# Optimization experiments

Measured on AMD Instinct MI355X. Metric: run time of the kernel, lower is better.

Reference implementation:

```python
import jax, jax.numpy as jnp
import numpy as np

D_MODEL = 768
D_STATE = 8
EXPAND = 2
D_HEAD = 64
D_CONV = 4
D_INNER = EXPAND * D_MODEL            # 1536
N_HEADS = D_INNER // D_HEAD           # 24
PARAM_DIM = 2                         # (A_freq, dt) per head per step
D_PROJ = 2 * D_INNER + N_HEADS * PARAM_DIM  # 3120
D_FF = 4 * D_MODEL
BATCH, SEQ = 2, 2048


def setup_inputs() -> dict:
    key = jax.random.key(0)
    ks = jax.random.split(key, 8)
    def s(k, shape, scale):
        return jax.random.normal(k, shape, dtype=jnp.float32) * scale
    return {
        "x": s(ks[0], (BATCH, SEQ, D_MODEL), 1.0),
        "norm1_w": jnp.ones((D_MODEL,), jnp.float32),
        "w_in": s(ks[1], (D_MODEL, D_PROJ), D_MODEL ** -0.5),
        "conv_w": s(ks[2], (D_INNER, D_CONV), D_CONV ** -0.5),
        "w_bc": s(ks[3], (D_INNER, 2 * N_HEADS * D_STATE), D_INNER ** -0.5),
        "D_skip": s(ks[4], (N_HEADS,), 1.0),
        "w_out": s(ks[5], (D_INNER, D_MODEL), D_INNER ** -0.5),
        "norm2_w": jnp.ones((D_MODEL,), jnp.float32),
        "ff_w1": s(ks[6], (D_MODEL, D_FF), D_MODEL ** -0.5),
        "ff_b1": jnp.zeros((D_FF,), jnp.float32),
        "ff_w2": s(ks[7], (D_FF, D_MODEL), D_FF ** -0.5),
        "ff_b2": jnp.zeros((D_MODEL,), jnp.float32),
    }


def _rmsnorm(x, w, eps=1e-6):
    return x * jax.lax.rsqrt(jnp.mean(x * x, axis=-1, keepdims=True) + eps) * w


def _l2norm(x, eps=1e-12):
    # normalize_bc=True: L2-normalize B/C rows over the state dim
    return x * jax.lax.rsqrt(jnp.sum(x * x, axis=-1, keepdims=True) + eps)


def _mixer(x, w_in, conv_w, w_bc, D_skip, w_out):
    Bsz, T, _ = x.shape
    proj = x @ w_in  # (B,T,3120)
    gate, vraw, params = jnp.split(proj, [D_INNER, 2 * D_INNER], axis=-1)
    # causal depthwise conv over time
    vpad = jnp.pad(vraw, ((0, 0), (D_CONV - 1, 0), (0, 0)))
    kernel = conv_w.T[:, None, :]  # (K, 1, C) for WIO, groups=C
    conv = jax.lax.conv_general_dilated(
        vpad, kernel, window_strides=(1,), padding='VALID',
        dimension_numbers=('NWC', 'WIO', 'NWC'), feature_group_count=D_INNER)
    v = jax.nn.silu(conv)  # (B,T,D_INNER)
    # B/C projections per head (normalized rows)
    bc = (v @ w_bc).reshape(Bsz, T, N_HEADS, 2, D_STATE)
    Bm = _l2norm(bc[..., 0, :])  # (B,T,H,N)
    Cm = _l2norm(bc[..., 1, :])  # (B,T,H,N)
    # LinOSS-IM discretizer: per-head time-varying frequency A and step dt
    p = params.reshape(Bsz, T, N_HEADS, PARAM_DIM)
    A = jax.nn.softplus(p[..., 0])
    dt = jax.nn.sigmoid(p[..., 1])
    S = 1.0 / (1.0 + dt * dt * A)  # implicit-midpoint Schur factor
    u = v.reshape(Bsz, T, N_HEADS, D_HEAD)
    tfirst = lambda a: jnp.moveaxis(a, 1, 0)

    def step(carry, inp):
        z, xs = carry  # each (B,H,N,P): velocity / position of the oscillator
        Bt, Ct, At, dtt, St, ut = inp
        d = dtt[..., None, None]
        a = At[..., None, None]
        s = St[..., None, None]
        bu = Bt[..., :, None] * ut[..., None, :]  # (B,H,N,P)
        z = s * (z - d * a * xs + d * bu)
        xs = xs + d * z
        y = jnp.einsum('bhn,bhnp->bhp', Ct, xs)
        return (z, xs), y

    z0 = jnp.zeros((Bsz, N_HEADS, D_STATE, D_HEAD), x.dtype)
    _, ys = jax.lax.scan(step, (z0, z0),
                         (tfirst(Bm), tfirst(Cm), tfirst(A), tfirst(dt), tfirst(S), tfirst(u)))
    y = jnp.moveaxis(ys, 0, 1)  # (B,T,H,P)
    # gate + per-head skip (D * u), then out projection
    gated = (y + D_skip[None, None, :, None] * u) * jax.nn.silu(gate).reshape(Bsz, T, N_HEADS, D_HEAD)
    return gated.reshape(Bsz, T, D_INNER) @ w_out


def reference(x, norm1_w, w_in, conv_w, w_bc, D_skip, w_out, norm2_w, ff_w1, ff_b1, ff_w2, ff_b2):
    x = x + _mixer(_rmsnorm(x, norm1_w), w_in, conv_w, w_bc, D_skip, w_out)
    h = _rmsnorm(x, norm2_w)
    return x + (jax.nn.gelu(h @ ff_w1 + ff_b1) @ ff_w2 + ff_b2)
```

## Files before the change

kernel.cpp:

```cpp
#include <hip/hip_runtime.h>

#define DMODEL 768
#define DINNER 1536
#define NHEADS 24
#define DHEAD  64
#define DSTATE 8
#define DPROJ  3120
#define DFF    3072
#define BATCH  2
#define SEQ    2048
#define BTTOT  (BATCH*SEQ)
#define NCHUNK 64
#define CT     32
#define NTBLK  8688

typedef unsigned short u16;
typedef __attribute__((ext_vector_type(8))) short bf16x8;
typedef __attribute__((ext_vector_type(4))) float f32x4;

__device__ __forceinline__ float b2f(u16 u){
  union { unsigned u; float f; } x; x.u = ((unsigned)u) << 16; return x.f;
}
__device__ __forceinline__ u16 f2b(float f){
  union { float f; unsigned u; } x; x.f = f;
  unsigned r = x.u + 0x7FFF + ((x.u >> 16) & 1);
  return (u16)(r >> 16);
}
__device__ __forceinline__ float ldin(const void* p, size_t i, bool f32){
  return f32 ? ((const float*)p)[i] : b2f(((const u16*)p)[i]);
}
__device__ __forceinline__ bool wire_f32(const u16* probe){ return probe[0] == 0; }

struct TDesc { const void* src; u16* dst; int R, C, bx, blk0; };
struct TPack { TDesc d[5]; };

__global__ __launch_bounds__(256) void pre_k(
    TPack P, const void* __restrict__ x, const void* __restrict__ w,
    u16* __restrict__ xn, const u16* __restrict__ probe)
{
  const bool f32 = wire_f32(probe);
  int bk = blockIdx.x;
  if (bk >= NTBLK){
    const size_t row = bk - NTBLK;
    float v[3]; float s = 0.f;
    #pragma unroll
    for (int i = 0; i < 3; i++){
      size_t idx = row * DMODEL + threadIdx.x + 256 * i;
      float f = ldin(x, idx, f32);
      v[i] = f; s += f * f;
    }
    #pragma unroll
    for (int o = 32; o > 0; o >>= 1) s += __shfl_xor(s, o);
    __shared__ float red[4];
    if ((threadIdx.x & 63) == 0) red[threadIdx.x >> 6] = s;
    __syncthreads();
    float tot = red[0] + red[1] + red[2] + red[3];
    float inv = rsqrtf(tot * (1.0f / DMODEL) + 1e-6f);
    #pragma unroll
    for (int i = 0; i < 3; i++){
      int c = threadIdx.x + 256 * i;
      xn[row * DMODEL + c] = f2b(v[i] * inv * ldin(w, c, f32));
    }
    return;
  }
  int s = 0;
  #pragma unroll
  for (int i = 1; i < 5; i++) if (bk >= P.d[i].blk0) s = i;
  const TDesc D = P.d[s];
  const int local = bk - D.blk0;
  const int cx = local % D.bx, ry = local / D.bx;
  const int c0 = cx * 32, r0 = ry * 32;
  const int R = D.R, C = D.C;
  __shared__ u16 tile[32][33];
  const int tx = threadIdx.x & 31, ty = threadIdx.x >> 5;
  #pragma unroll
  for (int i = 0; i < 32; i += 8){
    int r = r0 + ty + i, c = c0 + tx;
    u16 val = 0;
    if (r < R && c < C){
      size_t idx = (size_t)r * C + c;
      val = f32 ? f2b(((const float*)D.src)[idx]) : ((const u16*)D.src)[idx];
    }
    tile[ty + i][tx] = val;
  }
  __syncthreads();
  #pragma unroll
  for (int i = 0; i < 32; i += 8){
    int c = c0 + ty + i, r = r0 + tx;
    if (c < C && r < R) D.dst[(size_t)c * R + r] = tile[tx][ty + i];
  }
}

__global__ __launch_bounds__(256) void rmsnormW_k(
    const u16* __restrict__ pW, const void* __restrict__ x, const void* __restrict__ w,
    float* __restrict__ x2, u16* __restrict__ out, const u16* __restrict__ probe)
{
  const bool f32 = wire_f32(probe);
  const size_t row = blockIdx.x;
  const size_t MN = (size_t)BTTOT * DMODEL;
  float v[3]; float s = 0.f;
  #pragma unroll
  for (int i = 0; i < 3; i++){
    size_t idx = row * DMODEL + threadIdx.x + 256 * i;
    float f = ldin(x, idx, f32) + b2f(pW[idx]) + b2f(pW[MN + idx])
            + b2f(pW[2 * MN + idx]) + b2f(pW[3 * MN + idx]);
    x2[idx] = f;
    v[i] = f; s += f * f;
  }
  #pragma unroll
  for (int o = 32; o > 0; o >>= 1) s += __shfl_xor(s, o);
  __shared__ float red[4];
  if ((threadIdx.x & 63) == 0) red[threadIdx.x >> 6] = s;
  __syncthreads();
  float tot = red[0] + red[1] + red[2] + red[3];
  float inv = rsqrtf(tot * (1.0f / DMODEL) + 1e-6f);
  #pragma unroll
  for (int i = 0; i < 3; i++){
    int c = threadIdx.x + 256 * i;
    out[row * DMODEL + c] = f2b(v[i] * inv * ldin(w, c, f32));
  }
}

template <class Epi>
__global__ __launch_bounds__(256, 4) void gemm_bt(
    const u16* __restrict__ A, const u16* __restrict__ Bt,
    int M, int N, int Ks, int ldK, Epi epi, const u16* __restrict__ probe)
{
  const bool wf32 = wire_f32(probe);
  __shared__ __align__(16) u16 As[128 * 64];
  __shared__ __align__(16) u16 Bs[128 * 64];
  const int tid  = threadIdx.x;
  const int lane = tid & 63;
  const int wave = tid >> 6;
  const int wm = (wave >> 1) * 64;
  const int wn = (wave & 1) * 64;
  const int m0 = blockIdx.y * 128;
  const int n0 = blockIdx.x * 128;
  const int z  = blockIdx.z;
  const int kbase = z * Ks;
  const int rt = tid >> 3;
  const int cb = (tid & 7) * 8;
  const int sw = (rt & 7) * 8;

  f32x4 acc[4][4];
  const f32x4 z4 = {0.f, 0.f, 0.f, 0.f};
  #pragma unroll
  for (int i = 0; i < 4; i++)
    #pragma unroll
    for (int j = 0; j < 4; j++) acc[i][j] = z4;

  const int krow = lane & 15;
  const int kqo  = (lane >> 4) * 8;
  const int rsw  = (krow & 7) * 8;

  for (int k0 = kbase; k0 < kbase + Ks; k0 += 64){
    __syncthreads();
    #pragma unroll
    for (int i = 0; i < 4; i++){
      const u16* ga = A + ((size_t)(m0 + rt + 32 * i) * ldK + k0 + (cb ^ sw));
      __builtin_amdgcn_global_load_lds(
          (const __attribute__((address_space(1))) unsigned*)ga,
          (__attribute__((address_space(3))) unsigned*)(As + i * 2048 + wave * 512),
          16, 0, 0);
      int rb = n0 + rt + 32 * i; if (rb > N - 1) rb = N - 1;
      const u16* gb = Bt + ((size_t)rb * ldK + k0 + (cb ^ sw));
      __builtin_amdgcn_global_load_lds(
          (const __attribute__((address_space(1))) unsigned*)gb,
          (__attribute__((address_space(3))) unsigned*)(Bs + i * 2048 + wave * 512),
          16, 0, 0);
    }
    __syncthreads();
    #pragma unroll
    for (int ks = 0; ks < 2; ks++){
      const int koff = (ks * 32 + kqo) ^ rsw;
      bf16x8 af[4], bfr[4];
      #pragma unroll
      for (int i = 0; i < 4; i++){
        af[i]  = *(const bf16x8*)(As + (wm + i * 16 + krow) * 64 + koff);
        bfr[i] = *(const bf16x8*)(Bs + (wn + i * 16 + krow) * 64 + koff);
      }
      #pragma unroll
      for (int i = 0; i < 4; i++)
        #pragma unroll
        for (int j = 0; j < 4; j++)
          acc[i][j] = __builtin_amdgcn_mfma_f32_16x16x32_bf16(af[i], bfr[j], acc[i][j], 0, 0, 0);
    }
  }

  const int mb = m0 + wm + (lane >> 4) * 4;
  const int nb = n0 + wn + (lane & 15);
  #pragma unroll
  for (int i = 0; i < 4; i++)
    #pragma unroll
    for (int j = 0; j < 4; j++)
      #pragma unroll
      for (int r = 0; r < 4; r++){
        int m = mb + i * 16 + r;
        int n = nb + j * 16;
        if (n < N) epi(acc[i][j][r], m, n, wf32, z);
      }
}

struct EpiBf16 {
  u16* out; int ldo;
  __device__ void operator()(float v, int m, int n, bool, int) const {
    out[(size_t)m * ldo + n] = f2b(v);
  }
};
struct EpiPartB {
  u16* out; size_t ss; int ldo;
  __device__ void operator()(float v, int m, int n, bool, int z) const {
    out[(size_t)z * ss + (size_t)m * ldo + n] = f2b(v);
  }
};
struct EpiBiasGelu {
  u16* out; const void* bias; int ldo;
  __device__ void operator()(float v, int m, int n, bool f32, int) const {
    float x = v + ldin(bias, n, f32);
    float t = 0.7978845608028654f * (x + 0.044715f * x * x * x);
    out[(size_t)m * ldo + n] = f2b(0.5f * x * (1.0f + tanhf(t)));
  }
};

__global__ __launch_bounds__(256) void reduceF_k(
    const u16* __restrict__ pF, const void* __restrict__ bias,
    const float* __restrict__ x2, void* __restrict__ out,
    const u16* __restrict__ probe)
{
  const bool f32 = wire_f32(probe);
  const size_t MN = (size_t)BTTOT * DMODEL;
  size_t i = ((size_t)blockIdx.x * 256 + threadIdx.x) * 4;
  int n = (int)(i % DMODEL);
  float4 r = *(const float4*)(x2 + i);
  float o[4] = {r.x, r.y, r.z, r.w};
  #pragma unroll
  for (int k = 0; k < 4; k++){
    ushort4 p = *(const ushort4*)(pF + k * MN + i);
    o[0] += b2f(p.x); o[1] += b2f(p.y); o[2] += b2f(p.z); o[3] += b2f(p.w);
  }
  #pragma unroll
  for (int j = 0; j < 4; j++) o[j] += ldin(bias, n + j, f32);
  if (f32){
    *(float4*)((float*)out + i) = make_float4(o[0], o[1], o[2], o[3]);
  } else {
    u16* po = (u16*)out + i;
    po[0] = f2b(o[0]); po[1] = f2b(o[1]); po[2] = f2b(o[2]); po[3] = f2b(o[3]);
  }
}

__global__ __launch_bounds__(256) void conv_silu_k(
    const u16* __restrict__ proj, const void* __restrict__ cw, u16* __restrict__ v,
    const u16* __restrict__ probe)
{
  const bool f32 = wire_f32(probe);
  const int strip = blockIdx.x / 6;
  const int c = (blockIdx.x % 6) * 256 + threadIdx.x;
  const int bt0 = strip * 32;
  const bool head = (bt0 & (SEQ - 1)) == 0;
  const u16* base = proj + (size_t)bt0 * DPROJ + DINNER + c;
  const float w0 = ldin(cw, c * 4 + 0, f32), w1 = ldin(cw, c * 4 + 1, f32);
  const float w2 = ldin(cw, c * 4 + 2, f32), w3 = ldin(cw, c * 4 + 3, f32);
  float s0 = head ? 0.f : b2f(base[-3 * DPROJ]);
  float s1 = head ? 0.f : b2f(base[-2 * DPROJ]);
  float s2 = head ? 0.f : b2f(base[-1 * DPROJ]);
  u16* ov = v + (size_t)bt0 * DINNER + c;
  #pragma unroll
  for (int t = 0; t < 32; t++){
    float s3 = b2f(base[(size_t)t * DPROJ]);
    float a = fmaf(w0, s0, fmaf(w1, s1, fmaf(w2, s2, w3 * s3)));
    ov[(size_t)t * DINNER] = f2b(a / (1.f + __expf(-a)));
    s0 = s1; s1 = s2; s2 = s3;
  }
}

__global__ __launch_bounds__(256) void prep_k(
    const u16* __restrict__ proj, const u16* __restrict__ pB,
    float* __restrict__ bcn, float* __restrict__ prm)
{
  const size_t MNb = (size_t)BTTOT * 2 * NHEADS * DSTATE;
  int idx = blockIdx.x * 256 + threadIdx.x;
  if (idx >= BTTOT * NHEADS) return;
  int h = idx % NHEADS; int bt = idx / NHEADS;
  int b = bt >> 11, t = bt & (SEQ - 1);
  float p0 = b2f(proj[(size_t)bt * DPROJ + 2 * DINNER + h * 2]);
  float p1 = b2f(proj[(size_t)bt * DPROJ + 2 * DINNER + h * 2 + 1]);
  float A  = fmaxf(p0, 0.f) + log1pf(__expf(-fabsf(p0)));
  float dt = 1.f / (1.f + __expf(-p1));
  float S  = 1.f / (1.f + dt * dt * A);
  size_t pb = ((size_t)(b * NHEADS + h) * SEQ + t);
  float* pr = prm + pb * 4;
  pr[0] = S * dt * A; pr[1] = dt; pr[2] = S * dt; pr[3] = S;
  const u16* br = pB + (size_t)bt * (2 * NHEADS * DSTATE) + h * 16;
  float Bv[8] = {0,0,0,0,0,0,0,0}, Cv[8] = {0,0,0,0,0,0,0,0};
  #pragma unroll
  for (int k = 0; k < 8; k++){
    ushort4 b0 = *(const ushort4*)(br + k * MNb);
    ushort4 b1 = *(const ushort4*)(br + k * MNb + 4);
    ushort4 c0 = *(const ushort4*)(br + k * MNb + 8);
    ushort4 c1 = *(const ushort4*)(br + k * MNb + 12);
    Bv[0] += b2f(b0.x); Bv[1] += b2f(b0.y); Bv[2] += b2f(b0.z); Bv[3] += b2f(b0.w);
    Bv[4] += b2f(b1.x); Bv[5] += b2f(b1.y); Bv[6] += b2f(b1.z); Bv[7] += b2f(b1.w);
    Cv[0] += b2f(c0.x); Cv[1] += b2f(c0.y); Cv[2] += b2f(c0.z); Cv[3] += b2f(c0.w);
    Cv[4] += b2f(c1.x); Cv[5] += b2f(c1.y); Cv[6] += b2f(c1.z); Cv[7] += b2f(c1.w);
  }
  float sB = 1e-12f, sC = 1e-12f;
  #pragma unroll
  for (int j = 0; j < 8; j++){ sB += Bv[j] * Bv[j]; sC += Cv[j] * Cv[j]; }
  float rB = rsqrtf(sB), rC = rsqrtf(sC);
  float* o = bcn + pb * 16;
  #pragma unroll
  for (int j = 0; j < 8; j++){ o[j * 2] = Bv[j] * rB; o[j * 2 + 1] = Cv[j] * rC; }
}

__global__ __launch_bounds__(256) void scanA(
    const float* __restrict__ bcn, const float* __restrict__ prm,
    const u16* __restrict__ v, float2* __restrict__ rend, float4* __restrict__ phiE)
{
  if (blockIdx.x >= 768){
    int g = (blockIdx.x - 768) * 256 + threadIdx.x;
    if (g >= 48 * NCHUNK) return;
    const float4* pr = (const float4*)(prm + (size_t)g * CT * 4);
    float p00 = 1.f, p01 = 0.f, p10 = 0.f, p11 = 1.f;
    #pragma unroll 4
    for (int t = 0; t < CT; t++){
      float4 pv = pr[t];
      float n00 = pv.w * p00 - pv.x * p10;
      float n01 = pv.w * p01 - pv.x * p11;
      float n10 = fmaf(pv.z, p00, pv.w * p10);
      float n11 = fmaf(pv.z, p01, pv.w * p11);
      p00 = n00; p01 = n01; p10 = n10; p11 = n11;
    }
    phiE[g] = make_float4(p00, p01, p10, p11);
    return;
  }
  const int g = blockIdx.x * 4 + (threadIdx.x >> 6);
  const int bh = g >> 6, chunk = g & 63;
  const int b = bh / NHEADS, h = bh % NHEADS;
  const int t0 = chunk * CT;
  const int lane = threadIdx.x & 63;
  const float4* bcB = (const float4*)(bcn + ((size_t)bh * SEQ + t0) * 16);
  const float4* prB = (const float4*)(prm + ((size_t)bh * SEQ + t0) * 4);
  const u16* vB = v + ((size_t)b * SEQ + t0) * DINNER + h * DHEAD + lane;

  float z[8], xs[8];
  #pragma unroll
  for (int n = 0; n < 8; n++){ z[n] = 0.f; xs[n] = 0.f; }
  #pragma unroll 4
  for (int t = 0; t < CT; t++){
    float4 pv  = prB[t];
    float4 bc0 = bcB[t * 4 + 0], bc1 = bcB[t * 4 + 1];
    float4 bc2 = bcB[t * 4 + 2], bc3 = bcB[t * 4 + 3];
    float u = b2f(vB[(size_t)t * DINNER]);
    float Bv[8] = {bc0.x, bc0.z, bc1.x, bc1.z, bc2.x, bc2.z, bc3.x, bc3.z};
    #pragma unroll
    for (int n = 0; n < 8; n++){
      z[n]  = pv.w * z[n] - pv.x * xs[n] + pv.z * (Bv[n] * u);
      xs[n] = fmaf(pv.y, z[n], xs[n]);
    }
  }
  float2* rb = rend + (size_t)g * 512 + lane;
  #pragma unroll
  for (int n = 0; n < 8; n++) rb[n * 64] = make_float2(z[n], xs[n]);
}

__global__ __launch_bounds__(512) void scanB(
    const float2* __restrict__ rend, const float4* __restrict__ phiE,
    float2* __restrict__ s0)
{
  const int bh = blockIdx.x, tid = threadIdx.x;
  float z = 0.f, xs = 0.f;
  for (int c = 0; c < NCHUNK; c++){
    size_t idx = ((size_t)bh * NCHUNK + c) * 512 + tid;
    s0[idx] = make_float2(z, xs);
    float4 ph = phiE[bh * NCHUNK + c];
    float2 r  = rend[idx];
    float nz = ph.x * z + ph.y * xs + r.x;
    float nx = ph.z * z + ph.w * xs + r.y;
    z = nz; xs = nx;
  }
}

__global__ __launch_bounds__(256) void scanC(
    const float* __restrict__ bcn, const float* __restrict__ prm,
    const u16* __restrict__ v, const u16* __restrict__ proj,
    const float2* __restrict__ s0, const void* __restrict__ Dsk,
    u16* __restrict__ gated, const u16* __restrict__ probe)
{
  const bool f32 = wire_f32(probe);
  const int g = blockIdx.x * 4 + (threadIdx.x >> 6);
  const int bh = g >> 6, chunk = g & 63;
  const int b = bh / NHEADS, h = bh % NHEADS;
  const int t0 = chunk * CT;
  const int lane = threadIdx.x & 63;
  const float4* bcB = (const float4*)(bcn + ((size_t)bh * SEQ + t0) * 16);
  const float4* prB = (const float4*)(prm + ((size_t)bh * SEQ + t0) * 4);
  const u16* vB = v     + ((size_t)b * SEQ + t0) * DINNER + h * DHEAD + lane;
  const u16* gB = proj  + ((size_t)b * SEQ + t0) * DPROJ  + h * DHEAD + lane;
  u16*       oB = gated + ((size_t)b * SEQ + t0) * DINNER + h * DHEAD + lane;
  const float dsk = ldin(Dsk, h, f32);

  float z[8], xs[8];
  const float2* sb = s0 + (size_t)g * 512 + lane;
  #pragma unroll
  for (int n = 0; n < 8; n++){ float2 s = sb[n * 64]; z[n] = s.x; xs[n] = s.y; }
  #pragma unroll 4
  for (int t = 0; t < CT; t++){
    float4 pv  = prB[t];
    float4 bc0 = bcB[t * 4 + 0], bc1 = bcB[t * 4 + 1];
    float4 bc2 = bcB[t * 4 + 2], bc3 = bcB[t * 4 + 3];
    float u  = b2f(vB[(size_t)t * DINNER]);
    float gt = b2f(gB[(size_t)t * DPROJ]);
    float Bv[8] = {bc0.x, bc0.z, bc1.x, bc1.z, bc2.x, bc2.z, bc3.x, bc3.z};
    float Cv[8] = {bc0.y, bc0.w, bc1.y, bc1.w, bc2.y, bc2.w, bc3.y, bc3.w};
    float y = 0.f;
    #pragma unroll
    for (int n = 0; n < 8; n++){
      z[n]  = pv.w * z[n] - pv.x * xs[n] + pv.z * (Bv[n] * u);
      xs[n] = fmaf(pv.y, z[n], xs[n]);
      y     = fmaf(Cv[n], xs[n], y);
    }
    float sil = gt / (1.f + __expf(-gt));
    oB[(size_t)t * DINNER] = f2b((y + dsk * u) * sil);
  }
}

extern "C" void kernel_launch(void* const* d_in, const int* in_sizes, int n_in,
                              void* d_out, int out_size, void* d_ws, size_t ws_size,
                              hipStream_t stream)
{
  const void* x      = d_in[0];
  const u16*  probe  = (const u16*)d_in[1];
  const void* norm1w = d_in[1];
  const void* w_in   = d_in[2];
  const void* conv_w = d_in[3];
  const void* w_bc   = d_in[4];
  const void* Dsk    = d_in[5];
  const void* w_out  = d_in[6];
  const void* norm2w = d_in[7];
  const void* ff_w1  = d_in[8];
  const void* ff_b1  = d_in[9];
  const void* ff_w2  = d_in[10];
  const void* ff_b2  = d_in[11];

  char* wsb = (char*)d_ws;
  size_t off = 0;
  auto alloc = [&](size_t bytes) -> void* {
    void* p = wsb + off; off += (bytes + 255) & ~(size_t)255; return p;
  };
  u16*   w_inT  = (u16*)  alloc((size_t)DPROJ * DMODEL * 2);
  u16*   w_bcT  = (u16*)  alloc((size_t)(2 * NHEADS * DSTATE) * DINNER * 2);
  u16*   w_outT = (u16*)  alloc((size_t)DMODEL * DINNER * 2);
  u16*   ff_w1T = (u16*)  alloc((size_t)DFF * DMODEL * 2);
  u16*   ff_w2T = (u16*)  alloc((size_t)DMODEL * DFF * 2);
  u16*   xn     = (u16*)  alloc((size_t)BTTOT * DMODEL * 2);
  u16*   proj   = (u16*)  alloc((size_t)BTTOT * DPROJ * 2);
  u16*   v      = (u16*)  alloc((size_t)BTTOT * DINNER * 2);
  float* bcn    = (float*)alloc((size_t)48 * SEQ * 16 * 4);
  float* prm    = (float*)alloc((size_t)48 * SEQ * 4 * 4);
  u16*   gated  = (u16*)  alloc((size_t)BTTOT * DINNER * 2);
  float* x2     = (float*)alloc((size_t)BTTOT * DMODEL * 4);
  u16*   hbuf   = (u16*)  alloc((size_t)BTTOT * DMODEL * 2);
  float4* phiE  = (float4*)alloc((size_t)48 * NCHUNK * 16);
  char*  scrU   = (char*) alloc((size_t)27 * 1024 * 1024);
  u16*   pB     = (u16*)scrU;
  float2* rend  = (float2*)scrU;
  float2* s0b   = (float2*)(scrU + (size_t)48 * NCHUNK * 512 * 8);
  u16*   pF     = (u16*)scrU;
  u16*   pW     = proj;
  u16*   a1     = proj;

  TPack tp;
  tp.d[0] = {w_in,  w_inT,  DMODEL, DPROJ,               98, 0};
  tp.d[1] = {w_bc,  w_bcT,  DINNER, 2 * NHEADS * DSTATE, 12, 2352};
  tp.d[2] = {w_out, w_outT, DINNER, DMODEL,              24, 2928};
  tp.d[3] = {ff_w1, ff_w1T, DMODEL, DFF,                 96, 4080};
  tp.d[4] = {ff_w2, ff_w2T, DFF,    DMODEL,              24, 6384};
  pre_k<<<NTBLK + BTTOT, 256, 0, stream>>>(tp, x, norm1w, xn, probe);

  gemm_bt<<<dim3(25, 32, 1), 256, 0, stream>>>(xn, w_inT, BTTOT, DPROJ, DMODEL, DMODEL,
                                               EpiBf16{proj, DPROJ}, probe);
  conv_silu_k<<<768, 256, 0, stream>>>(proj, conv_w, v, probe);
  gemm_bt<<<dim3(3, 32, 8), 256, 0, stream>>>(v, w_bcT, BTTOT, 2 * NHEADS * DSTATE,
                                              1536 / 8, DINNER,
                                              EpiPartB{pB, (size_t)BTTOT * 2 * NHEADS * DSTATE, 2 * NHEADS * DSTATE}, probe);
  prep_k<<<(BTTOT * NHEADS) / 256, 256, 0, stream>>>(proj, pB, bcn, prm);

  scanA<<<780, 256, 0, stream>>>(bcn, prm, v, rend, phiE);
  scanB<<<48, 512, 0, stream>>>(rend, phiE, s0b);
  scanC<<<48 * NCHUNK / 4, 256, 0, stream>>>(bcn, prm, v, proj, s0b, Dsk, gated, probe);

  gemm_bt<<<dim3(6, 32, 4), 256, 0, stream>>>(gated, w_outT, BTTOT, DMODEL, 1536 / 4, DINNER,
                                              EpiPartB{pW, (size_t)BTTOT * DMODEL, DMODEL}, probe);
  rmsnormW_k<<<BTTOT, 256, 0, stream>>>(pW, x, norm2w, x2, hbuf, probe);
  gemm_bt<<<dim3(24, 32, 1), 256, 0, stream>>>(hbuf, ff_w1T, BTTOT, DFF, DMODEL, DMODEL,
                                               EpiBiasGelu{a1, ff_b1, DFF}, probe);
  gemm_bt<<<dim3(6, 32, 4), 256, 0, stream>>>(a1, ff_w2T, BTTOT, DMODEL, 3072 / 4, DFF,
                                              EpiPartB{pF, (size_t)BTTOT * DMODEL, DMODEL}, probe);
  reduceF_k<<<(BTTOT * DMODEL) / 1024, 256, 0, stream>>>(pF, ff_b2, x2, d_out, probe);
}
```

Before: 356.2 us.

## Double-buffer GEMM LDS tiles and raise FF2 split-K to 8

The bf16 MFMA GEMM now splits each K tile into two 32-wide LDS buffers with a matching XOR swizzle. The async global-to-LDS load of the next K slice is issued before the MFMAs on the current slice, so memory latency overlaps compute instead of being exposed between barriers. Separately, the FF2 GEMM split-K goes from 4 to 8 to launch more blocks. The reduction kernel now sums 8 partials, and the scratch buffer grows to hold them, which adds partial-sum write and read traffic. The loop needs an even number of 32-wide K steps, which holds for all current call sites.

Result: slower. 378.4 us (+6.2%).

```diff
diff --git a/kernel.cpp b/kernel.cpp
--- a/kernel.cpp
+++ b/kernel.cpp
@@ -127,8 +127,8 @@
     int M, int N, int Ks, int ldK, Epi epi, const u16* __restrict__ probe)
 {
   const bool wf32 = wire_f32(probe);
-  __shared__ __align__(16) u16 As[128 * 64];
-  __shared__ __align__(16) u16 Bs[128 * 64];
+  __shared__ __align__(16) u16 As[2][128 * 32];
+  __shared__ __align__(16) u16 Bs[2][128 * 32];
   const int tid  = threadIdx.x;
   const int lane = tid & 63;
   const int wave = tid >> 6;
@@ -136,11 +136,37 @@
   const int wn = (wave & 1) * 64;
   const int m0 = blockIdx.y * 128;
   const int n0 = blockIdx.x * 128;
-  const int z  = blockIdx.z;
-  const int kbase = z * Ks;
-  const int rt = tid >> 3;
-  const int cb = (tid & 7) * 8;
-  const int sw = (rt & 7) * 8;
+  const int kbase = blockIdx.z * Ks;
+
+  const int rl = lane >> 2, kc = lane & 3;
+  const int r0 = wave * 16 + rl;
+  const int r1 = r0 + 64;
+  const int sw0 = (kc ^ ((r0 >> 2) & 3)) * 8;
+  const int sw1 = (kc ^ ((r1 >> 2) & 3)) * 8;
+  int rbB0 = n0 + r0; if (rbB0 > N - 1) rbB0 = N - 1;
+  int rbB1 = n0 + r1; if (rbB1 > N - 1) rbB1 = N - 1;
+  const u16* gA0 = A  + (size_t)(m0 + r0) * ldK + kbase + sw0;
+  const u16* gA1 = A  + (size_t)(m0 + r1) * ldK + kbase + sw1;
+  const u16* gB0 = Bt + (size_t)rbB0 * ldK + kbase + sw0;
+  const u16* gB1 = Bt + (size_t)rbB1 * ldK + kbase + sw1;
+  const int lds0 = r0 * 32 + kc * 8;
+  const int lds1 = r1 * 32 + kc * 8;
+
+  auto stage = [&](int buf, int it){
+    const size_t ko = (size_t)it * 32;
+    __builtin_amdgcn_global_load_lds(
+        (const __attribute__((address_space(1))) unsigned*)(gA0 + ko),
+        (__attribute__((address_space(3))) unsigned*)(&As[buf][lds0]), 16, 0, 0);
+    __builtin_amdgcn_global_load_lds(
+        (const __attribute__((address_space(1))) unsigned*)(gA1 + ko),
+        (__attribute__((address_space(3))) unsigned*)(&As[buf][lds1]), 16, 0, 0);
+    __builtin_amdgcn_global_load_lds(
+        (const __attribute__((address_space(1))) unsigned*)(gB0 + ko),
+        (__attribute__((address_space(3))) unsigned*)(&Bs[buf][lds0]), 16, 0, 0);
+    __builtin_amdgcn_global_load_lds(
+        (const __attribute__((address_space(1))) unsigned*)(gB1 + ko),
+        (__attribute__((address_space(3))) unsigned*)(&Bs[buf][lds1]), 16, 0, 0);
+  };
 
   f32x4 acc[4][4];
   const f32x4 z4 = {0.f, 0.f, 0.f, 0.f};
@@ -150,41 +176,33 @@
     for (int j = 0; j < 4; j++) acc[i][j] = z4;
 
   const int krow = lane & 15;
-  const int kqo  = (lane >> 4) * 8;
-  const int rsw  = (krow & 7) * 8;
-
-  for (int k0 = kbase; k0 < kbase + Ks; k0 += 64){
+  const int fsw  = ((lane >> 4) ^ ((krow >> 2) & 3)) * 8;
+
+  auto compute = [&](int buf){
+    bf16x8 af[4], bfr[4];
+    #pragma unroll
+    for (int i = 0; i < 4; i++)
+      af[i]  = *(const bf16x8*)(&As[buf][(wm + i * 16 + krow) * 32 + fsw]);
+    #pragma unroll
+    for (int j = 0; j < 4; j++)
+      bfr[j] = *(const bf16x8*)(&Bs[buf][(wn + j * 16 + krow) * 32 + fsw]);
+    #pragma unroll
+    for (int i = 0; i < 4; i++)
+      #pragma unroll
+      for (int j = 0; j < 4; j++)
+        acc[i][j] = __builtin_amdgcn_mfma_f32_16x16x32_bf16(af[i], bfr[j], acc[i][j], 0, 0, 0);
+  };
+
+  const int NIT = Ks >> 5;
+  stage(0, 0);
+  __syncthreads();
+  for (int it = 0; it < NIT; it += 2){
+    if (it + 1 < NIT) stage(1, it + 1);
+    compute(0);
     __syncthreads();
-    #pragma unroll
-    for (int i = 0; i < 4; i++){
-      const u16* ga = A + ((size_t)(m0 + rt + 32 * i) * ldK + k0 + (cb ^ sw));
-      __builtin_amdgcn_global_load_lds(
-          (const __attribute__((address_space(1))) unsigned*)ga,
-          (__attribute__((address_space(3))) unsigned*)(As + i * 2048 + wave * 512),
-          16, 0, 0);
-      int rb = n0 + rt + 32 * i; if (rb > N - 1) rb = N - 1;
-      const u16* gb = Bt + ((size_t)rb * ldK + k0 + (cb ^ sw));
-      __builtin_amdgcn_global_load_lds(
-          (const __attribute__((address_space(1))) unsigned*)gb,
-          (__attribute__((address_space(3))) unsigned*)(Bs + i * 2048 + wave * 512),
-          16, 0, 0);
-    }
+    if (it + 2 < NIT) stage(0, it + 2);
+    compute(1);
     __syncthreads();
-    #pragma unroll
-    for (int ks = 0; ks < 2; ks++){
-      const int koff = (ks * 32 + kqo) ^ rsw;
-      bf16x8 af[4], bfr[4];
-      #pragma unroll
-      for (int i = 0; i < 4; i++){
-        af[i]  = *(const bf16x8*)(As + (wm + i * 16 + krow) * 64 + koff);
-        bfr[i] = *(const bf16x8*)(Bs + (wn + i * 16 + krow) * 64 + koff);
-      }
-      #pragma unroll
-      for (int i = 0; i < 4; i++)
-        #pragma unroll
-        for (int j = 0; j < 4; j++)
-          acc[i][j] = __builtin_amdgcn_mfma_f32_16x16x32_bf16(af[i], bfr[j], acc[i][j], 0, 0, 0);
-    }
   }
 
   const int mb = m0 + wm + (lane >> 4) * 4;
@@ -197,7 +215,7 @@
       for (int r = 0; r < 4; r++){
         int m = mb + i * 16 + r;
         int n = nb + j * 16;
-        if (n < N) epi(acc[i][j][r], m, n, wf32, z);
+        if (n < N) epi(acc[i][j][r], m, n, wf32, blockIdx.z);
       }
 }
 
@@ -234,7 +252,7 @@
   float4 r = *(const float4*)(x2 + i);
   float o[4] = {r.x, r.y, r.z, r.w};
   #pragma unroll
-  for (int k = 0; k < 4; k++){
+  for (int k = 0; k < 8; k++){
     ushort4 p = *(const ushort4*)(pF + k * MN + i);
     o[0] += b2f(p.x); o[1] += b2f(p.y); o[2] += b2f(p.z); o[3] += b2f(p.w);
   }
@@ -461,7 +479,7 @@
   float* x2     = (float*)alloc((size_t)BTTOT * DMODEL * 4);
   u16*   hbuf   = (u16*)  alloc((size_t)BTTOT * DMODEL * 2);
   float4* phiE  = (float4*)alloc((size_t)48 * NCHUNK * 16);
-  char*  scrU   = (char*) alloc((size_t)27 * 1024 * 1024);
+  char*  scrU   = (char*) alloc((size_t)52 * 1024 * 1024);
   u16*   pB     = (u16*)scrU;
   float2* rend  = (float2*)scrU;
   float2* s0b   = (float2*)(scrU + (size_t)48 * NCHUNK * 512 * 8);
@@ -494,7 +512,7 @@
   rmsnormW_k<<<BTTOT, 256, 0, stream>>>(pW, x, norm2w, x2, hbuf, probe);
   gemm_bt<<<dim3(24, 32, 1), 256, 0, stream>>>(hbuf, ff_w1T, BTTOT, DFF, DMODEL, DMODEL,
                                                EpiBiasGelu{a1, ff_b1, DFF}, probe);
-  gemm_bt<<<dim3(6, 32, 4), 256, 0, stream>>>(a1, ff_w2T, BTTOT, DMODEL, 3072 / 4, DFF,
+  gemm_bt<<<dim3(6, 32, 8), 256, 0, stream>>>(a1, ff_w2T, BTTOT, DMODEL, 3072 / 8, DFF,
                                               EpiPartB{pF, (size_t)BTTOT * DMODEL, DMODEL}, probe);
   reduceF_k<<<(BTTOT * DMODEL) / 1024, 256, 0, stream>>>(pF, ff_b2, x2, d_out, probe);
 }
```
